# Kernel optimization log

Hardware: AMD Instinct MI355X
Metric: run time of the kernel (lower is better)

## Reference

```python
import jax, jax.numpy as jnp
import numpy as np

B, T, D, H = 2, 2048, 1024, 16
HS = D // H  # head_size = 64
DFF = 4 * D


def setup_inputs() -> dict:
    key = jax.random.key(0)
    ks = jax.random.split(key, 12)
    s = 0.02
    return {
        "x": jax.random.normal(ks[0], (B, T, D), dtype=jnp.float32),
        "Wq": jax.random.normal(ks[1], (D, D), dtype=jnp.float32) * s,
        "Wk": jax.random.normal(ks[2], (D, D), dtype=jnp.float32) * s,
        "Wv": jax.random.normal(ks[3], (D, D), dtype=jnp.float32) * s,
        "Wo": jax.random.normal(ks[4], (D, D), dtype=jnp.float32) * s,
        "bo": jnp.zeros((D,), dtype=jnp.float32),
        "W1": jax.random.normal(ks[5], (D, DFF), dtype=jnp.float32) * s,
        "b1": jnp.zeros((DFF,), dtype=jnp.float32),
        "W2": jax.random.normal(ks[6], (DFF, D), dtype=jnp.float32) * s,
        "b2": jnp.zeros((D,), dtype=jnp.float32),
        "g1": jnp.ones((D,), dtype=jnp.float32),
        "be1": jnp.zeros((D,), dtype=jnp.float32),
        "g2": jnp.ones((D,), dtype=jnp.float32),
        "be2": jnp.zeros((D,), dtype=jnp.float32),
    }


def layer_norm(x, g, b, eps=1e-5):
    mu = jnp.mean(x, axis=-1, keepdims=True)
    var = jnp.var(x, axis=-1, keepdims=True)
    return (x - mu) * jax.lax.rsqrt(var + eps) * g + b


def attention(x, Wq, Wk, Wv, Wo, bo):
    # x: [B,T,D] -> q,k,v: [B,H,T,HS]
    def split_heads(y):
        return y.reshape(B, T, H, HS).transpose(0, 2, 1, 3)
    q = split_heads(x @ Wq)
    k = split_heads(x @ Wk)
    v = split_heads(x @ Wv)
    scores = jnp.einsum("bhqd,bhkd->bhqk", q, k) / jnp.sqrt(jnp.float32(HS))
    causal = jnp.tril(jnp.ones((T, T), dtype=bool))
    scores = jnp.where(causal, scores, -jnp.inf)
    probs = jax.nn.softmax(scores, axis=-1)
    out = jnp.einsum("bhqk,bhkd->bhqd", probs, v)
    out = out.transpose(0, 2, 1, 3).reshape(B, T, D)
    return out @ Wo + bo


def reference(x, Wq, Wk, Wv, Wo, bo, W1, b1, W2, b2, g1, be1, g2, be2):
    x = x + attention(layer_norm(x, g1, be1), Wq, Wk, Wv, Wo, bo)
    h = layer_norm(x, g2, be2)
    x = x + (jax.nn.relu(h @ W1 + b1) @ W2 + b2)
    return x
```

## Files before the change

### kernel.cpp

```cpp
#include <hip/hip_runtime.h>
#include <stdint.h>

#define Bc   2
#define Tc   2048
#define Dc   1024
#define Hc   16
#define HSc  64
#define DFFc 4096
#define Mc   (Bc * Tc)

using f32x4 = __attribute__((ext_vector_type(4))) float;
using s16x8 = __attribute__((ext_vector_type(8))) short;

__device__ __forceinline__ ushort f2bf(float f) {
  union { float f; uint32_t u; } v; v.f = f;
  uint32_t r = (v.u + 0x7FFFu + ((v.u >> 16) & 1u)) >> 16;
  return (ushort)r;
}
__device__ __forceinline__ float bf2f(ushort u) {
  union { uint32_t u; float f; } v; v.u = ((uint32_t)u) << 16;
  return v.f;
}
__device__ __forceinline__ uint32_t cvtpk(float a, float b) {
  uint32_t r;
  asm volatile("v_cvt_pk_bf16_f32 %0, %1, %2" : "=v"(r) : "v"(a), "v"(b));
  return r;
}
__device__ __forceinline__ float wredsum(float v) {
#pragma unroll
  for (int o = 32; o > 0; o >>= 1) v += __shfl_down(v, o);
  return v;
}

__device__ __forceinline__ void gload16(const ushort* g, ushort* l) {
  __builtin_amdgcn_global_load_lds(
      (const __attribute__((address_space(1))) void*)g,
      (__attribute__((address_space(3))) void*)l, 16, 0, 0);
}

template <int N> __device__ __forceinline__ void vwait() {
  if constexpr (N == 0) asm volatile("s_waitcnt vmcnt(0)" ::: "memory");
  else if constexpr (N == 3) asm volatile("s_waitcnt vmcnt(3)" ::: "memory");
  else if constexpr (N == 4) asm volatile("s_waitcnt vmcnt(4)" ::: "memory");
  else if constexpr (N == 6) asm volatile("s_waitcnt vmcnt(6)" ::: "memory");
  else asm volatile("s_waitcnt vmcnt(8)" ::: "memory");
}

__global__ __launch_bounds__(256) void tcast_all_kernel(
    const float* __restrict__ Wq, const float* __restrict__ Wk,
    const float* __restrict__ Wv, const float* __restrict__ Wo,
    const float* __restrict__ W1, const float* __restrict__ W2,
    ushort* __restrict__ wqkvt, ushort* __restrict__ wot,
    ushort* __restrict__ w1t, ushort* __restrict__ w2t) {
  __shared__ float t[32][33];
  const int id = blockIdx.x;
  const float* src; ushort* dst; int K, N, bx, by;
  if (id < 4096) {
    const int which = id >> 10, local = id & 1023;
    src = (which == 0) ? Wq : (which == 1) ? Wk : (which == 2) ? Wv : Wo;
    dst = (which == 3) ? wot : wqkvt + (size_t)which * 1024 * 1024;
    K = 1024; N = 1024; bx = local & 31; by = local >> 5;
  } else if (id < 8192) {
    const int local = id - 4096;
    src = W1; dst = w1t; K = 1024; N = 4096;
    bx = local & 127; by = local >> 7;
  } else {
    const int local = id - 8192;
    src = W2; dst = w2t; K = 4096; N = 1024;
    bx = local & 31; by = local >> 5;
  }
  const int tid = threadIdx.x;
  const int n0 = bx * 32, k0 = by * 32;
  const int r = tid >> 3, c4 = (tid & 7) * 4;
  const float4 v = *(const float4*)&src[(size_t)(k0 + r) * N + n0 + c4];
  t[r][c4] = v.x; t[r][c4 + 1] = v.y; t[r][c4 + 2] = v.z; t[r][c4 + 3] = v.w;
  __syncthreads();
  ushort4 o;
  o.x = f2bf(t[c4 + 0][r]); o.y = f2bf(t[c4 + 1][r]);
  o.z = f2bf(t[c4 + 2][r]); o.w = f2bf(t[c4 + 3][r]);
  *(ushort4*)&dst[(size_t)(n0 + r) * K + k0 + c4] = o;
}

__global__ __launch_bounds__(256) void ln_kernel(const float* __restrict__ x,
                                                 const float* __restrict__ g,
                                                 const float* __restrict__ b,
                                                 ushort* __restrict__ out) {
  const int row = blockIdx.x;
  const int tid = threadIdx.x;
  const int lane = tid & 63, wave = tid >> 6;
  const float4 v = ((const float4*)(x + (size_t)row * Dc))[tid];
  float s  = v.x + v.y + v.z + v.w;
  float s2 = v.x * v.x + v.y * v.y + v.z * v.z + v.w * v.w;
  __shared__ float rs[4], rs2[4];
  s = wredsum(s); s2 = wredsum(s2);
  if (lane == 0) { rs[wave] = s; rs2[wave] = s2; }
  __syncthreads();
  const float S  = rs[0] + rs[1] + rs[2] + rs[3];
  const float S2 = rs2[0] + rs2[1] + rs2[2] + rs2[3];
  const float mu = S * (1.f / (float)Dc);
  const float rstd = rsqrtf(S2 * (1.f / (float)Dc) - mu * mu + 1e-5f);
  const float4 gv = ((const float4*)g)[tid];
  const float4 bv = ((const float4*)b)[tid];
  ushort4 o;
  o.x = f2bf((v.x - mu) * rstd * gv.x + bv.x);
  o.y = f2bf((v.y - mu) * rstd * gv.y + bv.y);
  o.z = f2bf((v.z - mu) * rstd * gv.z + bv.z);
  o.w = f2bf((v.w - mu) * rstd * gv.w + bv.w);
  ((ushort4*)(out + (size_t)row * Dc))[tid] = o;
}

template <int BM, int NSPLIT, int OUT_BF16, int RELU, int BIAS, int RES, int QKVSPLIT>
__global__ __launch_bounds__(256) void gemm3_kernel(
    const ushort* __restrict__ A, const ushort* __restrict__ Bt,
    const float* __restrict__ bias, const float* __restrict__ res,
    void* __restrict__ C0, void* __restrict__ C1, void* __restrict__ C2,
    int M, int N, int K) {
  constexpr int MF = BM / 32;
  __shared__ __align__(16) ushort As[BM * 64];
  __shared__ __align__(16) ushort Bs[128 * 64];
  const int tid = threadIdx.x;
  const int lane = tid & 63, w = tid >> 6;
  const int wm = w >> 1, wn = w & 1;
  const int row0 = blockIdx.x * BM, col0 = blockIdx.y * 128;
  const int fr = lane & 15, fg = lane >> 4;
  const int kbeg = (NSPLIT > 1) ? blockIdx.z * (K / NSPLIT) : 0;
  const int kend = (NSPLIT > 1) ? kbeg + K / NSPLIT : K;

  f32x4 acc[MF][4] = {};

  for (int k0 = kbeg; k0 < kend; k0 += 64) {
#pragma unroll
    for (int i = 0; i < BM * 8 / 256; i++) {
      const int c = i * 256 + tid;
      const int r = c >> 3, j = c & 7;
      gload16(A + (size_t)(row0 + r) * K + k0 + ((j ^ (r & 7)) << 3),
              As + (i * 256 + w * 64) * 8);
    }
#pragma unroll
    for (int i = 0; i < 4; i++) {
      const int c = i * 256 + tid;
      const int r = c >> 3, j = c & 7;
      gload16(Bt + (size_t)(col0 + r) * K + k0 + ((j ^ (r & 7)) << 3),
              Bs + (i * 256 + w * 64) * 8);
    }
    __syncthreads();

#pragma unroll
    for (int kk = 0; kk < 2; kk++) {
      const int js = ((kk * 4 + fg) ^ (fr & 7)) << 3;
      s16x8 af[MF], bfr[4];
#pragma unroll
      for (int m = 0; m < MF; m++)
        af[m] = *(const s16x8*)&As[(wm * (BM / 2) + m * 16 + fr) * 64 + js];
#pragma unroll
      for (int n = 0; n < 4; n++)
        bfr[n] = *(const s16x8*)&Bs[(wn * 64 + n * 16 + fr) * 64 + js];
#pragma unroll
      for (int m = 0; m < MF; m++)
#pragma unroll
        for (int n = 0; n < 4; n++)
          acc[m][n] = __builtin_amdgcn_mfma_f32_16x16x32_bf16(af[m], bfr[n], acc[m][n], 0, 0, 0);
    }
    __syncthreads();
  }

  void* Cb = C0;
  int cbase = col0;
  if (QKVSPLIT) {
    const int which = col0 >> 10;
    Cb = (which == 0) ? C0 : (which == 1) ? C1 : C2;
    cbase = col0 & 1023;
  }
  const int NW = QKVSPLIT ? 1024 : N;
#pragma unroll
  for (int m = 0; m < MF; m++) {
#pragma unroll
    for (int n = 0; n < 4; n++) {
#pragma unroll
      for (int i = 0; i < 4; i++) {
        const int r = row0 + wm * (BM / 2) + m * 16 + fg * 4 + i;
        const int c = cbase + wn * 64 + n * 16 + fr;
        float v = acc[m][n][i];
        if (BIAS) v += bias[col0 - cbase + c];
        if (RELU) v = fmaxf(v, 0.f);
        if (RES)  v += res[(size_t)r * NW + c];
        if (OUT_BF16) ((ushort*)Cb)[(size_t)r * NW + c] = f2bf(v);
        else          ((float*)Cb)[(size_t)r * NW + c] = v;
      }
    }
  }
}

template <int BM, int NSPLIT, int OUT_BF16, int RELU, int BIAS, int RES, int QKVSPLIT>
__global__ __launch_bounds__(512, 2) void gemm8_kernel(
    const ushort* __restrict__ A, const ushort* __restrict__ Bt,
    const float* __restrict__ bias, const float* __restrict__ res,
    void* __restrict__ C0, void* __restrict__ C1, void* __restrict__ C2,
    int M, int N, int K) {
  constexpr int WR = BM / 2;
  constexpr int FI = WR / 16;
  constexpr int APASS = BM / 128;
  constexpr int LPS = APASS + 2;
  constexpr int SLOT = (BM + 256) * 32;
  __shared__ __align__(16) ushort lds[4 * SLOT];

  const int tid = threadIdx.x;
  const int lane = tid & 63, w = tid >> 6;
  const int wm = w >> 2, wn = w & 3;
  const int fr = lane & 15, fg = lane >> 4;

  const int GX = gridDim.x;
  const int nwg = GX * gridDim.y;
  const int lid = blockIdx.y * GX + blockIdx.x;
  const int wg = (lid & 7) * (nwg >> 3) + (lid >> 3);
  const int row0 = (wg % GX) * BM, col0 = (wg / GX) * 256;

  const int kbeg = (NSPLIT > 1) ? blockIdx.z * (K / NSPLIT) : 0;
  const int nt = (K / NSPLIT) / 32;

  const int scc = tid & 3;
  const int sr0 = tid >> 2;
  const int jswz = (scc ^ ((sr0 >> 1) & 3)) * 8;

  const ushort* gA = A + (size_t)(row0 + sr0) * K + kbeg + jswz;
  const ushort* gB = Bt + (size_t)(col0 + sr0) * K + kbeg + jswz;

  f32x4 acc[FI][4] = {};

  auto STAGE = [&](int slot) {
    ushort* ba = lds + slot * SLOT;
#pragma unroll
    for (int i = 0; i < APASS; ++i)
      gload16(gA + (size_t)(i * 128) * K, ba + (i * 512 + w * 64) * 8);
    ushort* bb = ba + BM * 32;
#pragma unroll
    for (int i = 0; i < 2; ++i)
      gload16(gB + (size_t)(i * 128) * K, bb + (i * 512 + w * 64) * 8);
    gA += 32; gB += 32;
  };

  STAGE(0); STAGE(1); STAGE(2);
  vwait<2 * LPS>();
  __builtin_amdgcn_sched_barrier(0);
  __builtin_amdgcn_s_barrier();
  __builtin_amdgcn_sched_barrier(0);

  for (int sb = 0; sb < nt; sb += 4) {
#pragma unroll
    for (int u = 0; u < 4; ++u) {
      const int s = sb + u;
      const ushort* sa = lds + u * SLOT;
      const ushort* sbp = sa + BM * 32;
      s16x8 af[4], bf[4];
#pragma unroll
      for (int ni = 0; ni < 4; ++ni) {
        const int rb = wn * 64 + ni * 16 + fr;
        bf[ni] = *(const s16x8*)&sbp[rb * 32 + (fg ^ ((rb >> 1) & 3)) * 8];
      }
#pragma unroll
      for (int mi = 0; mi < 4; ++mi) {
        const int ra = wm * WR + mi * 16 + fr;
        af[mi] = *(const s16x8*)&sa[ra * 32 + (fg ^ ((ra >> 1) & 3)) * 8];
      }
      if (s + 3 < nt) STAGE((u + 3) & 3);
      __builtin_amdgcn_sched_barrier(0);
      __builtin_amdgcn_s_barrier();
      __builtin_amdgcn_sched_barrier(0);
      __builtin_amdgcn_s_setprio(1);
#pragma unroll
      for (int mi = 0; mi < 4; ++mi)
#pragma unroll
        for (int ni = 0; ni < 4; ++ni)
          acc[mi][ni] = __builtin_amdgcn_mfma_f32_16x16x32_bf16(
              af[mi], bf[ni], acc[mi][ni], 0, 0, 0);
      __builtin_amdgcn_s_setprio(0);
      if constexpr (FI == 8) {
#pragma unroll
        for (int mi = 0; mi < 4; ++mi) {
          const int ra = wm * WR + 64 + mi * 16 + fr;
          af[mi] = *(const s16x8*)&sa[ra * 32 + (fg ^ ((ra >> 1) & 3)) * 8];
        }
        __builtin_amdgcn_s_setprio(1);
#pragma unroll
        for (int mi = 0; mi < 4; ++mi)
#pragma unroll
          for (int ni = 0; ni < 4; ++ni)
            acc[4 + mi][ni] = __builtin_amdgcn_mfma_f32_16x16x32_bf16(
                af[mi], bf[ni], acc[4 + mi][ni], 0, 0, 0);
        __builtin_amdgcn_s_setprio(0);
      }
      __builtin_amdgcn_sched_barrier(0);
      {
        const int rem = nt - 2 - s;
        if (rem >= 2) vwait<2 * LPS>();
        else if (rem == 1) vwait<LPS>();
        else if (rem == 0) vwait<0>();
      }
      __builtin_amdgcn_s_barrier();
      __builtin_amdgcn_sched_barrier(0);
    }
  }

  __syncthreads();
  ushort* wst = lds + w * (WR * 64);
#pragma unroll
  for (int mi = 0; mi < FI; ++mi) {
#pragma unroll
    for (int ni = 0; ni < 4; ++ni) {
#pragma unroll
      for (int i = 0; i < 4; ++i) {
        float v = acc[mi][ni][i];
        if (NSPLIT == 1) {
          if (BIAS) v += bias[col0 + wn * 64 + ni * 16 + fr];
          if (RELU) v = fmaxf(v, 0.f);
        }
        wst[(mi * 16 + fg * 4 + i) * 64 + ni * 16 + fr] = f2bf(v);
      }
    }
  }
  const int rr = lane >> 3, cc = (lane & 7) * 8;
  if constexpr (NSPLIT > 1) {
    ushort* P = (ushort*)C0 + (size_t)blockIdx.z * M * N;
#pragma unroll
    for (int it = 0; it < WR / 8; ++it) {
      const int r = it * 8 + rr;
      *(uint4*)&P[(size_t)(row0 + wm * WR + r) * N + col0 + wn * 64 + cc] =
          *(const uint4*)&wst[r * 64 + cc];
    }
  } else {
    void* Cb = C0;
    int cbase = col0;
    if (QKVSPLIT) {
      const int which = col0 >> 10;
      Cb = (which == 0) ? C0 : (which == 1) ? C1 : C2;
      cbase = col0 & 1023;
    }
    const int NW = QKVSPLIT ? 1024 : N;
#pragma unroll
    for (int it = 0; it < WR / 8; ++it) {
      const int r = it * 8 + rr;
      *(uint4*)&((ushort*)Cb)[(size_t)(row0 + wm * WR + r) * NW + cbase + wn * 64 + cc] =
          *(const uint4*)&wst[r * 64 + cc];
    }
  }
}

__global__ __launch_bounds__(256) void sum2b_kernel(const ushort* __restrict__ p,
                                                    const float* __restrict__ bias,
                                                    const float* __restrict__ res,
                                                    float* __restrict__ out) {
  const size_t i = ((size_t)blockIdx.x * 256 + threadIdx.x) * 4;
  const size_t MN = (size_t)Mc * Dc;
  const ushort4 a = *(const ushort4*)(p + i);
  const ushort4 b = *(const ushort4*)(p + MN + i);
  const float4 r = *(const float4*)(res + i);
  const float4 bs = *(const float4*)(bias + (i & 1023));
  float4 o;
  o.x = bf2f(a.x) + bf2f(b.x) + bs.x + r.x;
  o.y = bf2f(a.y) + bf2f(b.y) + bs.y + r.y;
  o.z = bf2f(a.z) + bf2f(b.z) + bs.z + r.z;
  o.w = bf2f(a.w) + bf2f(b.w) + bs.w + r.w;
  *(float4*)(out + i) = o;
}

__global__ __launch_bounds__(512) void fattn3_kernel(const ushort* __restrict__ Q,
                                                     const ushort* __restrict__ K,
                                                     const ushort* __restrict__ V,
                                                     float* __restrict__ pacc,
                                                     float* __restrict__ pl) {
  __shared__ __align__(16) ushort Kl[2][64][72];
  __shared__ __align__(16) ushort Vt[2][64][72];
  __shared__ __align__(16) uint32_t Pu[8][512];

  const int tid = threadIdx.x;
  const int lane = tid & 63, w = tid >> 6;
  const int fr = lane & 15, fg = lane >> 4;

  const int bh   = blockIdx.x & 31;
  const int rest = blockIdx.x >> 5;
  const int qb   = 15 - (rest >> 1);
  const int z    = rest & 1;
  const int h = bh & 15, b = bh >> 4;
  const int q0 = qb * 128;
  const size_t hbase = (size_t)b * Tc * Dc + (size_t)h * HSc;

  s16x8 qf0, qf1;
  {
    const ushort* qp = Q + hbase + (size_t)(q0 + w * 16 + fr) * Dc + fg * 8;
    qf0 = *(const s16x8*)(qp);
    qf1 = *(const s16x8*)(qp + 32);
  }

  const int kkey = tid >> 3, kd8 = (tid & 7) * 8;
  const int vkey = tid & 63, vd8 = (tid >> 6) * 8;

  const int t0 = z * (qb + 1), t1 = (z + 1) * (qb + 1);
  uint4 kreg = *(const uint4*)(K + hbase + (size_t)(t0 * 64 + kkey) * Dc + kd8);
  uint4 vreg = *(const uint4*)(V + hbase + (size_t)(t0 * 64 + vkey) * Dc + vd8);

  f32x4 acc[4] = {};
  float ps = 0.f;
  const float Cs = 0.18033688f;

  for (int kt = t0; kt < t1; kt++) {
    const int cur = (kt - t0) & 1;
    *(uint4*)&Kl[cur][kkey][kd8] = kreg;
    {
      union { uint4 v; ushort u[8]; } t; t.v = vreg;
#pragma unroll
      for (int j = 0; j < 8; j++) Vt[cur][vd8 + j][vkey] = t.u[j];
    }
    if (kt + 1 < t1) {
      kreg = *(const uint4*)(K + hbase + (size_t)((kt + 1) * 64 + kkey) * Dc + kd8);
      vreg = *(const uint4*)(V + hbase + (size_t)((kt + 1) * 64 + vkey) * Dc + vd8);
    }
    __syncthreads();

    const bool skip = (kt * 64 > q0 + w * 16 + 15);
    if (!skip) {
      f32x4 s[4] = {};
      __builtin_amdgcn_s_setprio(1);
#pragma unroll
      for (int kf = 0; kf < 4; kf++) {
        const s16x8 k0 = *(const s16x8*)&Kl[cur][kf * 16 + fr][fg * 8];
        const s16x8 k1 = *(const s16x8*)&Kl[cur][kf * 16 + fr][32 + fg * 8];
        s[kf] = __builtin_amdgcn_mfma_f32_16x16x32_bf16(k0, qf0, s[kf], 0, 0, 0);
        s[kf] = __builtin_amdgcn_mfma_f32_16x16x32_bf16(k1, qf1, s[kf], 0, 0, 0);
      }
      __builtin_amdgcn_s_setprio(0);

      const bool diag = (kt * 64 + 63 > q0 + w * 16);
      const int qg = q0 + w * 16 + fr;
#pragma unroll
      for (int kf = 0; kf < 4; kf++) {
        float p[4];
#pragma unroll
        for (int i = 0; i < 4; i++) {
          p[i] = exp2f(s[kf][i] * Cs);
          if (diag) {
            const int kg = kt * 64 + kf * 16 + fg * 4 + i;
            if (kg > qg) p[i] = 0.f;
          }
          ps += p[i];
        }
        uint2 pk;
        pk.x = cvtpk(p[0], p[1]);
        pk.y = cvtpk(p[2], p[3]);
        *(uint2*)&Pu[w][(2 * kf + (fg >> 1)) * 64 + fr * 4 + (fg & 1) * 2] = pk;
      }

      const s16x8 pa0 = *(const s16x8*)&Pu[w][fg * 64 + fr * 4];
      const s16x8 pa1 = *(const s16x8*)&Pu[w][(4 + fg) * 64 + fr * 4];
      __builtin_amdgcn_s_setprio(1);
#pragma unroll
      for (int df = 0; df < 4; df++) {
        const s16x8 v0 = *(const s16x8*)&Vt[cur][df * 16 + fr][fg * 8];
        const s16x8 v1 = *(const s16x8*)&Vt[cur][df * 16 + fr][32 + fg * 8];
        acc[df] = __builtin_amdgcn_mfma_f32_16x16x32_bf16(pa0, v0, acc[df], 0, 0, 0);
        acc[df] = __builtin_amdgcn_mfma_f32_16x16x32_bf16(pa1, v1, acc[df], 0, 0, 0);
      }
      __builtin_amdgcn_s_setprio(0);
    }
  }

  ps += __shfl_xor(ps, 16);
  ps += __shfl_xor(ps, 32);
  if (lane < 16)
    pl[(size_t)z * (32 * 2048) + (size_t)bh * 2048 + q0 + w * 16 + lane] = ps;

  float* pa = pacc + (size_t)z * (32ull * 2048 * 64) + (size_t)bh * 2048 * 64;
#pragma unroll
  for (int i = 0; i < 4; i++) {
    const int qr = q0 + w * 16 + fg * 4 + i;
#pragma unroll
    for (int df = 0; df < 4; df++)
      pa[(size_t)qr * 64 + df * 16 + fr] = acc[df][i];
  }
}

__global__ __launch_bounds__(256) void amerge_kernel(const float* __restrict__ pacc,
                                                     const float* __restrict__ pl,
                                                     ushort* __restrict__ O) {
  const int g = blockIdx.x * 256 + threadIdx.x;
  const int d4 = g & 15;
  const int t  = (g >> 4) & 2047;
  const int bh = g >> 15;
  const int h = bh & 15, b = bh >> 4;
  const size_t base = ((size_t)bh * 2048 + t) * 64 + d4 * 4;
  const float4 a = *(const float4*)(pacc + base);
  const float4 c = *(const float4*)(pacc + 32ull * 2048 * 64 + base);
  const float inv = 1.f / (pl[(size_t)bh * 2048 + t] + pl[32 * 2048 + (size_t)bh * 2048 + t]);
  ushort4 o;
  o.x = f2bf((a.x + c.x) * inv);
  o.y = f2bf((a.y + c.y) * inv);
  o.z = f2bf((a.z + c.z) * inv);
  o.w = f2bf((a.w + c.w) * inv);
  *(ushort4*)&O[((size_t)(b * 2048 + t)) * 1024 + h * 64 + d4 * 4] = o;
}

extern "C" void kernel_launch(void* const* d_in, const int* in_sizes, int n_in,
                              void* d_out, int out_size, void* d_ws, size_t ws_size,
                              hipStream_t stream) {
  const float* x   = (const float*)d_in[0];
  const float* Wq  = (const float*)d_in[1];
  const float* Wk  = (const float*)d_in[2];
  const float* Wv  = (const float*)d_in[3];
  const float* Wo  = (const float*)d_in[4];
  const float* bo  = (const float*)d_in[5];
  const float* W1  = (const float*)d_in[6];
  const float* b1  = (const float*)d_in[7];
  const float* W2  = (const float*)d_in[8];
  const float* b2  = (const float*)d_in[9];
  const float* g1  = (const float*)d_in[10];
  const float* be1 = (const float*)d_in[11];
  const float* g2  = (const float*)d_in[12];
  const float* be2 = (const float*)d_in[13];

  char* ws = (char*)d_ws;
  const size_t MB = 1ull << 20;
  ushort* ln1   = (ushort*)(ws + 0 * MB);
  ushort* qb    = (ushort*)(ws + 8 * MB);
  ushort* kb    = (ushort*)(ws + 16 * MB);
  ushort* vb    = (ushort*)(ws + 24 * MB);
  ushort* wqkvt = (ushort*)(ws + 32 * MB);
  ushort* wot   = (ushort*)(ws + 38 * MB);
  ushort* w1t   = (ushort*)(ws + 40 * MB);
  ushort* w2t   = (ushort*)(ws + 48 * MB);
  float*  x1    = (float*)(ws + 56 * MB);
  ushort* hb    = (ushort*)(ws + 72 * MB);
  float*  pacc  = (float*)(ws + 56 * MB);
  float*  plv   = (float*)(ws + 88 * MB);
  ushort* fpart = (ushort*)(ws + 0 * MB);

  tcast_all_kernel<<<12288, 256, 0, stream>>>(Wq, Wk, Wv, Wo, W1, W2,
                                              wqkvt, wot, w1t, w2t);

  ln_kernel<<<Mc, 256, 0, stream>>>(x, g1, be1, ln1);

  gemm8_kernel<128, 1, 1, 0, 0, 0, 1><<<dim3(32, 12), 512, 0, stream>>>(
      ln1, wqkvt, nullptr, nullptr, qb, kb, vb, Mc, 3072, Dc);

  fattn3_kernel<<<1024, 512, 0, stream>>>(qb, kb, vb, pacc, plv);
  amerge_kernel<<<4096, 256, 0, stream>>>(pacc, plv, ln1);

  gemm3_kernel<64, 1, 0, 0, 1, 1, 0><<<dim3(64, 8), 256, 0, stream>>>(
      ln1, wot, bo, x, x1, nullptr, nullptr, Mc, Dc, Dc);

  ln_kernel<<<Mc, 256, 0, stream>>>(x1, g2, be2, qb);

  gemm8_kernel<256, 1, 1, 1, 1, 0, 0><<<dim3(16, 16), 512, 0, stream>>>(
      qb, w1t, b1, nullptr, hb, nullptr, nullptr, Mc, DFFc, Dc);

  gemm8_kernel<128, 2, 0, 0, 0, 0, 0><<<dim3(32, 4, 2), 512, 0, stream>>>(
      hb, w2t, nullptr, nullptr, fpart, nullptr, nullptr, Mc, Dc, DFFc);
  sum2b_kernel<<<4096, 256, 0, stream>>>(fpart, b2, x1, (float*)d_out);
}
```

Baseline: 214.4 us.

## Replace 8-wave GEMM with 4-wave 128x128 tile kernel and triple buffering

Replaces the 512-thread GEMM (BM x 256 tiles, 4-slot LDS ring, prefetch depth 3) with a 256-thread kernel using fixed 128x128 tiles, a 3-slot LDS ring and prefetch depth 2. The QKV, FFN1 and split-K FFN2 launches get correspondingly larger grids. The aim is more workgroups for better CU occupancy and load balance on the 256-CU part, with less LDS per block. The cost is lower per-tile data reuse, so more global and LDS traffic per FLOP, plus a shallower pipeline to hide latency.

```diff
diff --git a/kernel.cpp b/kernel.cpp
--- a/kernel.cpp
+++ b/kernel.cpp
@@ -191,120 +191,98 @@
   }
 }
 
-template <int BM, int NSPLIT, int OUT_BF16, int RELU, int BIAS, int RES, int QKVSPLIT>
-__global__ __launch_bounds__(512, 2) void gemm8_kernel(
+template <int NSPLIT, int OUT_BF16, int RELU, int BIAS, int RES, int QKVSPLIT>
+__global__ __launch_bounds__(256) void gemm10_kernel(
     const ushort* __restrict__ A, const ushort* __restrict__ Bt,
     const float* __restrict__ bias, const float* __restrict__ res,
     void* __restrict__ C0, void* __restrict__ C1, void* __restrict__ C2,
     int M, int N, int K) {
-  constexpr int WR = BM / 2;
-  constexpr int FI = WR / 16;
-  constexpr int APASS = BM / 128;
-  constexpr int LPS = APASS + 2;
-  constexpr int SLOT = (BM + 256) * 32;
-  __shared__ __align__(16) ushort lds[4 * SLOT];
+  constexpr int LPS = 4;
+  constexpr int SLOT = 256 * 32;
+  __shared__ __align__(16) ushort lds[3 * SLOT];
 
   const int tid = threadIdx.x;
   const int lane = tid & 63, w = tid >> 6;
-  const int wm = w >> 2, wn = w & 3;
+  const int wm = w >> 1, wn = w & 1;
   const int fr = lane & 15, fg = lane >> 4;
 
   const int GX = gridDim.x;
   const int nwg = GX * gridDim.y;
   const int lid = blockIdx.y * GX + blockIdx.x;
   const int wg = (lid & 7) * (nwg >> 3) + (lid >> 3);
-  const int row0 = (wg % GX) * BM, col0 = (wg / GX) * 256;
+  const int row0 = (wg % GX) * 128, col0 = (wg / GX) * 128;
 
   const int kbeg = (NSPLIT > 1) ? blockIdx.z * (K / NSPLIT) : 0;
   const int nt = (K / NSPLIT) / 32;
 
-  const int scc = tid & 3;
-  const int sr0 = tid >> 2;
+  const int sr0 = tid >> 2, scc = tid & 3;
   const int jswz = (scc ^ ((sr0 >> 1) & 3)) * 8;
 
   const ushort* gA = A + (size_t)(row0 + sr0) * K + kbeg + jswz;
   const ushort* gB = Bt + (size_t)(col0 + sr0) * K + kbeg + jswz;
 
-  f32x4 acc[FI][4] = {};
+  f32x4 acc[4][4] = {};
 
   auto STAGE = [&](int slot) {
     ushort* ba = lds + slot * SLOT;
 #pragma unroll
-    for (int i = 0; i < APASS; ++i)
-      gload16(gA + (size_t)(i * 128) * K, ba + (i * 512 + w * 64) * 8);
-    ushort* bb = ba + BM * 32;
-#pragma unroll
     for (int i = 0; i < 2; ++i)
-      gload16(gB + (size_t)(i * 128) * K, bb + (i * 512 + w * 64) * 8);
+      gload16(gA + (size_t)(i * 64) * K, ba + (i * 256 + w * 64) * 8);
+    ushort* bb = ba + 128 * 32;
+#pragma unroll
+    for (int i = 0; i < 2; ++i)
+      gload16(gB + (size_t)(i * 64) * K, bb + (i * 256 + w * 64) * 8);
     gA += 32; gB += 32;
   };
 
-  STAGE(0); STAGE(1); STAGE(2);
-  vwait<2 * LPS>();
+  STAGE(0); STAGE(1);
+  vwait<LPS>();
   __builtin_amdgcn_sched_barrier(0);
   __builtin_amdgcn_s_barrier();
   __builtin_amdgcn_sched_barrier(0);
 
-  for (int sb = 0; sb < nt; sb += 4) {
-#pragma unroll
-    for (int u = 0; u < 4; ++u) {
-      const int s = sb + u;
-      const ushort* sa = lds + u * SLOT;
-      const ushort* sbp = sa + BM * 32;
-      s16x8 af[4], bf[4];
-#pragma unroll
-      for (int ni = 0; ni < 4; ++ni) {
-        const int rb = wn * 64 + ni * 16 + fr;
-        bf[ni] = *(const s16x8*)&sbp[rb * 32 + (fg ^ ((rb >> 1) & 3)) * 8];
-      }
-#pragma unroll
-      for (int mi = 0; mi < 4; ++mi) {
-        const int ra = wm * WR + mi * 16 + fr;
-        af[mi] = *(const s16x8*)&sa[ra * 32 + (fg ^ ((ra >> 1) & 3)) * 8];
-      }
-      if (s + 3 < nt) STAGE((u + 3) & 3);
-      __builtin_amdgcn_sched_barrier(0);
-      __builtin_amdgcn_s_barrier();
-      __builtin_amdgcn_sched_barrier(0);
-      __builtin_amdgcn_s_setprio(1);
-#pragma unroll
-      for (int mi = 0; mi < 4; ++mi)
-#pragma unroll
-        for (int ni = 0; ni < 4; ++ni)
-          acc[mi][ni] = __builtin_amdgcn_mfma_f32_16x16x32_bf16(
-              af[mi], bf[ni], acc[mi][ni], 0, 0, 0);
-      __builtin_amdgcn_s_setprio(0);
-      if constexpr (FI == 8) {
-#pragma unroll
-        for (int mi = 0; mi < 4; ++mi) {
-          const int ra = wm * WR + 64 + mi * 16 + fr;
-          af[mi] = *(const s16x8*)&sa[ra * 32 + (fg ^ ((ra >> 1) & 3)) * 8];
-        }
-        __builtin_amdgcn_s_setprio(1);
-#pragma unroll
-        for (int mi = 0; mi < 4; ++mi)
-#pragma unroll
-          for (int ni = 0; ni < 4; ++ni)
-            acc[4 + mi][ni] = __builtin_amdgcn_mfma_f32_16x16x32_bf16(
-                af[mi], bf[ni], acc[4 + mi][ni], 0, 0, 0);
-        __builtin_amdgcn_s_setprio(0);
-      }
-      __builtin_amdgcn_sched_barrier(0);
-      {
-        const int rem = nt - 2 - s;
-        if (rem >= 2) vwait<2 * LPS>();
-        else if (rem == 1) vwait<LPS>();
-        else if (rem == 0) vwait<0>();
-      }
-      __builtin_amdgcn_s_barrier();
-      __builtin_amdgcn_sched_barrier(0);
-    }
+  int cur = 0, nxt = 2;
+  for (int s = 0; s < nt; ++s) {
+    const ushort* sa = lds + cur * SLOT;
+    const ushort* sbp = sa + 128 * 32;
+    s16x8 af[4], bf[4];
+#pragma unroll
+    for (int mi = 0; mi < 4; ++mi) {
+      const int ra = wm * 64 + mi * 16 + fr;
+      af[mi] = *(const s16x8*)&sa[ra * 32 + (fg ^ ((ra >> 1) & 3)) * 8];
+    }
+#pragma unroll
+    for (int ni = 0; ni < 4; ++ni) {
+      const int rb = wn * 64 + ni * 16 + fr;
+      bf[ni] = *(const s16x8*)&sbp[rb * 32 + (fg ^ ((rb >> 1) & 3)) * 8];
+    }
+    if (s + 2 < nt) STAGE(nxt);
+    __builtin_amdgcn_sched_barrier(0);
+    __builtin_amdgcn_s_barrier();
+    __builtin_amdgcn_sched_barrier(0);
+    __builtin_amdgcn_s_setprio(1);
+#pragma unroll
+    for (int mi = 0; mi < 4; ++mi)
+#pragma unroll
+      for (int ni = 0; ni < 4; ++ni)
+        acc[mi][ni] = __builtin_amdgcn_mfma_f32_16x16x32_bf16(
+            af[mi], bf[ni], acc[mi][ni], 0, 0, 0);
+    __builtin_amdgcn_s_setprio(0);
+    __builtin_amdgcn_sched_barrier(0);
+    {
+      if (s + 2 < nt) vwait<LPS>();
+      else if (s + 1 < nt) vwait<0>();
+    }
+    __builtin_amdgcn_s_barrier();
+    __builtin_amdgcn_sched_barrier(0);
+    cur = (cur == 2) ? 0 : cur + 1;
+    nxt = (nxt == 2) ? 0 : nxt + 1;
   }
 
   __syncthreads();
-  ushort* wst = lds + w * (WR * 64);
-#pragma unroll
-  for (int mi = 0; mi < FI; ++mi) {
+  ushort* wst = lds + w * (64 * 64);
+#pragma unroll
+  for (int mi = 0; mi < 4; ++mi) {
 #pragma unroll
     for (int ni = 0; ni < 4; ++ni) {
 #pragma unroll
@@ -318,13 +296,14 @@
       }
     }
   }
+  __builtin_amdgcn_s_barrier();
   const int rr = lane >> 3, cc = (lane & 7) * 8;
   if constexpr (NSPLIT > 1) {
     ushort* P = (ushort*)C0 + (size_t)blockIdx.z * M * N;
 #pragma unroll
-    for (int it = 0; it < WR / 8; ++it) {
+    for (int it = 0; it < 8; ++it) {
       const int r = it * 8 + rr;
-      *(uint4*)&P[(size_t)(row0 + wm * WR + r) * N + col0 + wn * 64 + cc] =
+      *(uint4*)&P[(size_t)(row0 + wm * 64 + r) * N + col0 + wn * 64 + cc] =
           *(const uint4*)&wst[r * 64 + cc];
     }
   } else {
@@ -337,9 +316,9 @@
     }
     const int NW = QKVSPLIT ? 1024 : N;
 #pragma unroll
-    for (int it = 0; it < WR / 8; ++it) {
+    for (int it = 0; it < 8; ++it) {
       const int r = it * 8 + rr;
-      *(uint4*)&((ushort*)Cb)[(size_t)(row0 + wm * WR + r) * NW + cbase + wn * 64 + cc] =
+      *(uint4*)&((ushort*)Cb)[(size_t)(row0 + wm * 64 + r) * NW + cbase + wn * 64 + cc] =
           *(const uint4*)&wst[r * 64 + cc];
     }
   }
@@ -537,7 +516,7 @@
 
   ln_kernel<<<Mc, 256, 0, stream>>>(x, g1, be1, ln1);
 
-  gemm8_kernel<128, 1, 1, 0, 0, 0, 1><<<dim3(32, 12), 512, 0, stream>>>(
+  gemm10_kernel<1, 1, 0, 0, 0, 1><<<dim3(32, 24), 256, 0, stream>>>(
       ln1, wqkvt, nullptr, nullptr, qb, kb, vb, Mc, 3072, Dc);
 
   fattn3_kernel<<<1024, 512, 0, stream>>>(qb, kb, vb, pacc, plv);
@@ -548,10 +527,10 @@
 
   ln_kernel<<<Mc, 256, 0, stream>>>(x1, g2, be2, qb);
 
-  gemm8_kernel<256, 1, 1, 1, 1, 0, 0><<<dim3(16, 16), 512, 0, stream>>>(
+  gemm10_kernel<1, 1, 1, 1, 0, 0><<<dim3(32, 32), 256, 0, stream>>>(
       qb, w1t, b1, nullptr, hb, nullptr, nullptr, Mc, DFFc, Dc);
 
-  gemm8_kernel<128, 2, 0, 0, 0, 0, 0><<<dim3(32, 4, 2), 512, 0, stream>>>(
+  gemm10_kernel<2, 0, 0, 0, 0, 0><<<dim3(32, 8, 2), 256, 0, stream>>>(
       hb, w2t, nullptr, nullptr, fpart, nullptr, nullptr, Mc, Dc, DFFc);
   sum2b_kernel<<<4096, 256, 0, stream>>>(fpart, b2, x1, (float*)d_out);
 }
```

Measured after the change: 225.6 us. 5.2% more time.
